# Optimization experiments

Hardware: AMD Instinct MI355X
Metric: run time of the kernel (lower is better)

## Reference

```python
import jax, jax.numpy as jnp
import numpy as np

N_NODES = 50000
N_EDGES = 800000
IN_F = 128
HID = 16
HEADS = 8
OUT_F = 128


def setup_inputs() -> dict:
    key = jax.random.key(0)
    ks = jax.random.split(key, 16)
    h = jax.random.normal(ks[0], (N_NODES, IN_F), dtype=jnp.float32)
    src1 = jax.random.randint(ks[1], (N_EDGES,), 0, N_NODES, dtype=jnp.int32)
    dst1 = jax.random.randint(ks[2], (N_EDGES,), 0, N_NODES, dtype=jnp.int32)
    src2 = jax.random.randint(ks[3], (N_EDGES,), 0, N_NODES, dtype=jnp.int32)
    dst2 = jax.random.randint(ks[4], (N_EDGES,), 0, N_NODES, dtype=jnp.int32)
    norm1 = jax.random.uniform(ks[5], (N_NODES, 1), dtype=jnp.float32)
    norm2 = jax.random.uniform(ks[6], (N_NODES, 1), dtype=jnp.float32)
    D = HEADS * HID  # 128
    W_lin = jax.random.normal(ks[7], (IN_F, D), dtype=jnp.float32) * (1.0 / np.sqrt(IN_F))
    b_lin = jax.random.normal(ks[8], (D,), dtype=jnp.float32) * 0.01
    al = jax.random.normal(ks[9], (HEADS, HID, 1), dtype=jnp.float32) * 0.1
    ar = jax.random.normal(ks[10], (HEADS, HID, 1), dtype=jnp.float32) * 0.1
    W_fc = jax.random.normal(ks[11], (D, OUT_F), dtype=jnp.float32) * (1.0 / np.sqrt(D))
    b_fc = jax.random.normal(ks[12], (OUT_F,), dtype=jnp.float32) * 0.01
    return {"h": h, "src1": src1, "dst1": dst1, "src2": src2, "dst2": dst2,
            "norm1": norm1, "norm2": norm2, "W_lin": W_lin, "b_lin": b_lin,
            "al": al, "ar": ar, "W_fc": W_fc, "b_fc": b_fc}


def _propagate(feat, norm, src, dst, n_nodes):
    # msg = h[src] * norm[src]; accum[v] = sum_{e: dst=v} msg_e; out = accum * norm
    msg = feat[src] * norm[src]                      # [E, D]
    agg = jax.ops.segment_sum(msg, dst, num_segments=n_nodes)
    return agg * norm                                # [N, D]


def _leaky_relu(x):
    return jnp.where(x > 0, x, 0.2 * x)


def reference(h, src1, dst1, src2, dst2, norm1, norm2, W_lin, b_lin, al, ar, W_fc, b_fc):
    N = h.shape[0]
    hf = h @ W_lin + b_lin                           # [N, 8*HID] (dropout p given but eval-mode -> identity)
    h1 = _propagate(hf, norm1, src1, dst1, N)
    h2 = _propagate(hf, norm2, src2, dst2, N)
    # Faithful to torch: row-major reshape [N, 8*HID] -> (8, N, HID)
    h1r = h1.reshape(HEADS, N, HID)
    h2r = h2.reshape(HEADS, N, HID)
    hr = hf.reshape(HEADS, N, HID)
    ai = jnp.einsum('hnd,hdo->hno', hr, al)          # [8, N, 1]
    aj1 = jnp.einsum('hnd,hdo->hno', h1r, ar)
    aj2 = jnp.einsum('hnd,hdo->hno', h2r, ar)
    a1 = jnp.clip(jnp.exp(_leaky_relu(ai + aj1)), -10.0, 10.0)
    a2 = jnp.clip(jnp.exp(_leaky_relu(ai + aj2)), -10.0, 10.0)
    denom = a1 + a2
    out = (a1 / denom) * h1r + (a2 / denom) * h2r    # [8, N, HID]
    out = out.reshape(N, HEADS * HID)
    return out @ W_fc + b_fc
```

## Files before the change

kernel.cpp:

```cpp
#include <hip/hip_runtime.h>

#define NN 50000
#define NE 800000
#define NB 196
#define NBLK 512
#define CHUNK 1563
#define MAXB 6144

typedef __bf16 bf16x8 __attribute__((ext_vector_type(8)));
typedef float  f32x4  __attribute__((ext_vector_type(4)));

__device__ __forceinline__ unsigned short f2bf(float x) {
    unsigned u = __float_as_uint(x);
    return (unsigned short)((u + 0x7FFFu + ((u >> 16) & 1u)) >> 16);
}
__device__ __forceinline__ float bflo(unsigned u) { return __uint_as_float(u << 16); }
__device__ __forceinline__ float bfhi(unsigned u) { return __uint_as_float(u & 0xFFFF0000u); }

__global__ __launch_bounds__(256) void convert_w_kernel(
    const float* __restrict__ Wa, const float* __restrict__ Wb,
    unsigned short* __restrict__ Wta, unsigned short* __restrict__ Wtb)
{
    __shared__ float ls[128 * 132];
    const float* W = blockIdx.x ? Wb : Wa;
    unsigned short* Wt = blockIdx.x ? Wtb : Wta;
    const int t = threadIdx.x;
    for (int i = t; i < 128 * 32; i += 256) {
        int k = i >> 5, n4 = i & 31;
        *(float4*)&ls[k * 132 + n4 * 4] = ((const float4*)W)[i];
    }
    __syncthreads();
    for (int j = t; j < 128 * 128; j += 256) {
        int n = j >> 7, k = j & 127;
        Wt[j] = f2bf(ls[k * 132 + n]);
    }
}

__global__ __launch_bounds__(256) void mfma_gemm_kernel(
    const float* __restrict__ X, const unsigned short* __restrict__ Wt,
    const float* __restrict__ bias, float* __restrict__ Y,
    unsigned short* __restrict__ Ybf, int nrows)
{
    __shared__ unsigned short Wl[128 * 128];
    const int t = threadIdx.x;
    const int lane = t & 63;
    const int wv = t >> 6;
    const int row0 = blockIdx.x * 64;
    const int m16 = lane & 15;
    const int quad = lane >> 4;

    {
        const uint4* Wg = (const uint4*)Wt;
        #pragma unroll
        for (int i = 0; i < 8; i++) {
            int gi = t + i * 256;
            int n = gi >> 4, g = gi & 15;
            uint4 v = Wg[gi];
            *(uint4*)&Wl[n * 128 + (((g ^ (n & 15)) << 3))] = v;
        }
    }

    const int arow = row0 + wv * 16 + m16;
    const bool valid = (arow < nrows);
    const float4* X4 = (const float4*)X;
    float4 xr[8];
    #pragma unroll
    for (int kc = 0; kc < 4; kc++) {
        if (valid) {
            int gidx = arow * 32 + kc * 8 + quad * 2;
            xr[kc * 2]     = X4[gidx];
            xr[kc * 2 + 1] = X4[gidx + 1];
        } else {
            xr[kc * 2] = xr[kc * 2 + 1] = make_float4(0.f, 0.f, 0.f, 0.f);
        }
    }
    __syncthreads();

    f32x4 acc[8];
    #pragma unroll
    for (int nt = 0; nt < 8; nt++) acc[nt] = (f32x4){0.f, 0.f, 0.f, 0.f};

    #pragma unroll
    for (int kc = 0; kc < 4; kc++) {
        union { unsigned short u[8]; bf16x8 v; } ah, al;
        float f[8] = { xr[kc*2].x, xr[kc*2].y, xr[kc*2].z, xr[kc*2].w,
                       xr[kc*2+1].x, xr[kc*2+1].y, xr[kc*2+1].z, xr[kc*2+1].w };
        #pragma unroll
        for (int j = 0; j < 8; j++) {
            unsigned u = __float_as_uint(f[j]);
            ah.u[j] = (unsigned short)(u >> 16);
            al.u[j] = f2bf(f[j] - __uint_as_float(u & 0xFFFF0000u));
        }
        const int sgbase = (kc * 4 + quad);
        #pragma unroll
        for (int nt = 0; nt < 8; nt++) {
            const int n = nt * 16 + m16;
            bf16x8 b = *(const bf16x8*)&Wl[n * 128 + ((sgbase ^ m16) << 3)];
            acc[nt] = __builtin_amdgcn_mfma_f32_16x16x32_bf16(ah.v, b, acc[nt], 0, 0, 0);
            acc[nt] = __builtin_amdgcn_mfma_f32_16x16x32_bf16(al.v, b, acc[nt], 0, 0, 0);
        }
    }

    #pragma unroll
    for (int nt = 0; nt < 8; nt++) {
        const int col = nt * 16 + m16;
        const float bc = bias[col];
        #pragma unroll
        for (int r = 0; r < 4; r++) {
            int row = row0 + wv * 16 + quad * 4 + r;
            if (row < nrows) {
                float val = acc[nt][r] + bc;
                if (Y)   Y[(long)row * 128 + col] = val;
                if (Ybf) Ybf[(long)row * 128 + col] = f2bf(val);
            }
        }
    }
}

__global__ __launch_bounds__(256) void histA_kernel(
    const int* __restrict__ dst1, const int* __restrict__ dst2, int* __restrict__ histG)
{
    __shared__ int h[2 * NB];
    const int t = threadIdx.x, blk = blockIdx.x;
    for (int i = t; i < 2 * NB; i += 256) h[i] = 0;
    __syncthreads();
    const int base = blk * CHUNK;
    const int lim = min(CHUNK, NE - base);
    for (int i = t; i < lim; i += 256) {
        atomicAdd(&h[dst1[base + i] >> 8], 1);
        atomicAdd(&h[NB + (dst2[base + i] >> 8)], 1);
    }
    __syncthreads();
    for (int i = t; i < 2 * NB; i += 256)
        histG[(size_t)i * NBLK + blk] = h[i];
}

__global__ __launch_bounds__(512) void scanB1_kernel(int* __restrict__ histG, int* __restrict__ btot)
{
    __shared__ int s[NBLK];
    const int t = threadIdx.x, row = blockIdx.x;
    int v = histG[(size_t)row * NBLK + t];
    s[t] = v;
    __syncthreads();
    for (int off = 1; off < NBLK; off <<= 1) {
        int x = (t >= off) ? s[t - off] : 0;
        __syncthreads();
        s[t] += x;
        __syncthreads();
    }
    histG[(size_t)row * NBLK + t] = s[t] - v;
    if (t == NBLK - 1) btot[row] = s[t];
}

__global__ __launch_bounds__(256) void scanB2_kernel(const int* __restrict__ btot, int* __restrict__ bbase)
{
    __shared__ int sc[256];
    const int t = threadIdx.x;
    for (int g = 0; g < 2; g++) {
        int v = (t < NB) ? btot[g * NB + t] : 0;
        sc[t] = v;
        __syncthreads();
        for (int off = 1; off < 256; off <<= 1) {
            int x = (t >= off) ? sc[t - off] : 0;
            __syncthreads();
            sc[t] += x;
            __syncthreads();
        }
        if (t < NB) bbase[g * NB + t] = sc[t] - v;
        __syncthreads();
    }
}

__global__ __launch_bounds__(256) void scatterC_kernel(
    const int* __restrict__ src1, const int* __restrict__ dst1,
    const int* __restrict__ src2, const int* __restrict__ dst2,
    const int* __restrict__ histG, const int* __restrict__ bbase,
    unsigned int* __restrict__ bin1, unsigned int* __restrict__ bin2)
{
    __shared__ int pos[2 * NB];
    const int t = threadIdx.x, blk = blockIdx.x;
    for (int i = t; i < 2 * NB; i += 256)
        pos[i] = bbase[i] + histG[(size_t)i * NBLK + blk];
    __syncthreads();
    const int base = blk * CHUNK;
    const int lim = min(CHUNK, NE - base);
    for (int i = t; i < lim; i += 256) {
        int d = dst1[base + i], s = src1[base + i];
        int slot = atomicAdd(&pos[d >> 8], 1);
        bin1[slot] = ((unsigned)(d & 255) << 16) | (unsigned)s;
        d = dst2[base + i]; s = src2[base + i];
        slot = atomicAdd(&pos[NB + (d >> 8)], 1);
        bin2[slot] = ((unsigned)(d & 255) << 16) | (unsigned)s;
    }
}

__global__ __launch_bounds__(256) void bucket_sort_kernel(
    const unsigned int* __restrict__ bin1, const unsigned int* __restrict__ bin2,
    const int* __restrict__ bbase, const int* __restrict__ btot,
    unsigned short* __restrict__ csr1, int* __restrict__ start1, int* __restrict__ deg1,
    unsigned short* __restrict__ csr2, int* __restrict__ start2, int* __restrict__ deg2)
{
    __shared__ int lcnt[256];
    __shared__ int sc[256];
    __shared__ int oat[256];
    __shared__ unsigned short outb[MAXB];
    const int t = threadIdx.x;
    const int g = (blockIdx.x >= NB) ? 1 : 0;
    const int b = blockIdx.x - g * NB;
    const unsigned int* bin = g ? bin2 : bin1;
    unsigned short* csr = g ? csr2 : csr1;
    int* start = g ? start2 : start1;
    int* deg   = g ? deg2 : deg1;

    const int base = bbase[g * NB + b];
    const int tot = min(btot[g * NB + b], MAXB);

    lcnt[t] = 0;
    __syncthreads();
    for (int i = t; i < tot; i += 256) atomicAdd(&lcnt[bin[base + i] >> 16], 1);
    __syncthreads();
    sc[t] = lcnt[t];
    __syncthreads();
    for (int off = 1; off < 256; off <<= 1) {
        int x = (t >= off) ? sc[t - off] : 0;
        __syncthreads();
        sc[t] += x;
        __syncthreads();
    }
    const int ex = sc[t] - lcnt[t];
    oat[t] = ex;
    __syncthreads();
    for (int i = t; i < tot; i += 256) {
        unsigned v = bin[base + i];
        int slot = atomicAdd(&oat[v >> 16], 1);
        outb[slot] = (unsigned short)(v & 0xFFFFu);
    }
    __syncthreads();
    for (int i = t; i < tot; i += 256) csr[base + i] = outb[i];
    int nd = b * 256 + t;
    if (nd < NN) { start[nd] = base + ex; deg[nd] = lcnt[t]; }
}

__global__ __launch_bounds__(256) void gather_both_kernel(
    const unsigned int* __restrict__ hfb,
    const unsigned short* __restrict__ csr1, const int* __restrict__ start1,
    const int* __restrict__ deg1, const float* __restrict__ norm1, float* __restrict__ agg1,
    const unsigned short* __restrict__ csr2, const int* __restrict__ start2,
    const int* __restrict__ deg2, const float* __restrict__ norm2, float* __restrict__ agg2)
{
    int w = (blockIdx.x * 256 + threadIdx.x) >> 6;
    int lane = threadIdx.x & 63;
    if (w >= 2 * NN) return;
    const int g = (w >= NN);
    const int node = w - g * NN;
    const unsigned short* csr = g ? csr2 : csr1;
    const int* start = g ? start2 : start1;
    const int* deg   = g ? deg2 : deg1;
    const float* norm = g ? norm2 : norm1;
    float* agg = g ? agg2 : agg1;

    int st = start[node];
    int dg = deg[node];
    float2 acc = make_float2(0.f, 0.f);
    int i = 0;
    for (; i + 4 <= dg; i += 4) {
        int s0 = csr[st + i], s1 = csr[st + i + 1], s2 = csr[st + i + 2], s3 = csr[st + i + 3];
        float n0 = norm[s0], n1 = norm[s1], n2 = norm[s2], n3 = norm[s3];
        unsigned u0 = hfb[(long)s0 * 64 + lane];
        unsigned u1 = hfb[(long)s1 * 64 + lane];
        unsigned u2 = hfb[(long)s2 * 64 + lane];
        unsigned u3 = hfb[(long)s3 * 64 + lane];
        acc.x = fmaf(bflo(u0), n0, acc.x); acc.y = fmaf(bfhi(u0), n0, acc.y);
        acc.x = fmaf(bflo(u1), n1, acc.x); acc.y = fmaf(bfhi(u1), n1, acc.y);
        acc.x = fmaf(bflo(u2), n2, acc.x); acc.y = fmaf(bfhi(u2), n2, acc.y);
        acc.x = fmaf(bflo(u3), n3, acc.x); acc.y = fmaf(bfhi(u3), n3, acc.y);
    }
    for (; i < dg; i++) {
        int s = csr[st + i];
        float nv = norm[s];
        unsigned u = hfb[(long)s * 64 + lane];
        acc.x = fmaf(bflo(u), nv, acc.x); acc.y = fmaf(bfhi(u), nv, acc.y);
    }
    ((float2*)agg)[(long)node * 64 + lane] = acc;
}

__global__ __launch_bounds__(256) void attention_kernel(
    const unsigned int* __restrict__ hfb, float* __restrict__ agg1,
    const float* __restrict__ agg2, const float* __restrict__ norm1,
    const float* __restrict__ norm2, const float* __restrict__ al,
    const float* __restrict__ ar)
{
    int gid = blockIdx.x * 256 + threadIdx.x;
    int m = gid >> 2;
    int j = gid & 3;
    if (m >= 8 * NN) return;
    int n = m >> 3;
    int head = m / NN;
    float n1 = norm1[n], n2v = norm2[n];
    uint2 u = ((const uint2*)hfb)[gid];
    float4 f = make_float4(bflo(u.x), bfhi(u.x), bflo(u.y), bfhi(u.y));
    float4 g1 = ((const float4*)agg1)[gid];
    float4 g2 = ((const float4*)agg2)[gid];
    g1.x *= n1; g1.y *= n1; g1.z *= n1; g1.w *= n1;
    g2.x *= n2v; g2.y *= n2v; g2.z *= n2v; g2.w *= n2v;
    float4 av = ((const float4*)al)[head * 4 + j];
    float4 rv = ((const float4*)ar)[head * 4 + j];
    float s_ai = f.x * av.x + f.y * av.y + f.z * av.z + f.w * av.w;
    float s1 = g1.x * rv.x + g1.y * rv.y + g1.z * rv.z + g1.w * rv.w;
    float s2 = g2.x * rv.x + g2.y * rv.y + g2.z * rv.z + g2.w * rv.w;
    s_ai += __shfl_xor(s_ai, 1); s_ai += __shfl_xor(s_ai, 2);
    s1   += __shfl_xor(s1, 1);   s1   += __shfl_xor(s1, 2);
    s2   += __shfl_xor(s2, 1);   s2   += __shfl_xor(s2, 2);
    float x1 = s_ai + s1; x1 = x1 > 0.f ? x1 : 0.2f * x1;
    float x2 = s_ai + s2; x2 = x2 > 0.f ? x2 : 0.2f * x2;
    float e1 = fminf(expf(x1), 10.f);
    float e2 = fminf(expf(x2), 10.f);
    float inv = 1.f / (e1 + e2);
    float w1 = e1 * inv, w2 = e2 * inv;
    float4 o;
    o.x = w1 * g1.x + w2 * g2.x;
    o.y = w1 * g1.y + w2 * g2.y;
    o.z = w1 * g1.z + w2 * g2.z;
    o.w = w1 * g1.w + w2 * g2.w;
    ((float4*)agg1)[gid] = o;
}

extern "C" void kernel_launch(void* const* d_in, const int* in_sizes, int n_in,
                              void* d_out, int out_size, void* d_ws, size_t ws_size,
                              hipStream_t stream)
{
    const float* h     = (const float*)d_in[0];
    const int*   src1  = (const int*)  d_in[1];
    const int*   dst1  = (const int*)  d_in[2];
    const int*   src2  = (const int*)  d_in[3];
    const int*   dst2  = (const int*)  d_in[4];
    const float* norm1 = (const float*)d_in[5];
    const float* norm2 = (const float*)d_in[6];
    const float* W_lin = (const float*)d_in[7];
    const float* b_lin = (const float*)d_in[8];
    const float* al    = (const float*)d_in[9];
    const float* ar    = (const float*)d_in[10];
    const float* W_fc  = (const float*)d_in[11];
    const float* b_fc  = (const float*)d_in[12];
    float* out = (float*)d_out;

    float* agg1 = (float*)d_ws;
    float* agg2 = agg1 + (size_t)NN * 128;
    unsigned int* bin1 = (unsigned int*)agg2;
    unsigned int* bin2 = bin1 + NE;
    unsigned short* hfb  = (unsigned short*)(agg2 + (size_t)NN * 128);
    unsigned short* csr1 = hfb + (size_t)NN * 128;
    unsigned short* csr2 = csr1 + NE;
    unsigned short* WtL  = csr2 + NE;
    unsigned short* WtF  = WtL + 128 * 128;
    int* histG  = (int*)(WtF + 128 * 128);
    int* btot   = histG + 2 * NB * NBLK;
    int* bbase  = btot + 2 * NB;
    int* start1 = bbase + 2 * NB;
    int* start2 = start1 + NN;
    int* deg1   = start2 + NN;
    int* deg2   = deg1 + NN;

    convert_w_kernel<<<2, 256, 0, stream>>>(W_lin, W_fc, WtL, WtF);

    mfma_gemm_kernel<<<(NN + 63) / 64, 256, 0, stream>>>(h, WtL, b_lin, nullptr, hfb, NN);

    histA_kernel<<<NBLK, 256, 0, stream>>>(dst1, dst2, histG);
    scanB1_kernel<<<2 * NB, NBLK, 0, stream>>>(histG, btot);
    scanB2_kernel<<<1, 256, 0, stream>>>(btot, bbase);
    scatterC_kernel<<<NBLK, 256, 0, stream>>>(src1, dst1, src2, dst2, histG, bbase, bin1, bin2);
    bucket_sort_kernel<<<2 * NB, 256, 0, stream>>>(bin1, bin2, bbase, btot,
                                                   csr1, start1, deg1,
                                                   csr2, start2, deg2);

    gather_both_kernel<<<(2 * NN * 64 + 255) / 256, 256, 0, stream>>>(
        (const unsigned int*)hfb,
        csr1, start1, deg1, norm1, agg1,
        csr2, start2, deg2, norm2, agg2);

    attention_kernel<<<8 * NN * 4 / 256, 256, 0, stream>>>((const unsigned int*)hfb, agg1, agg2,
                                                           norm1, norm2, al, ar);

    mfma_gemm_kernel<<<(NN + 63) / 64, 256, 0, stream>>>(agg1, WtF, b_fc, out, nullptr, NN);
}
```

Before: 262.1 us.

## Fuse gather with attention and feed bf16 output to single-pass GEMM

Merges the two-graph gather and the attention step into one kernel, where one wavefront handles a node for both graphs. CSR indices are loaded cooperatively and broadcast with readlane. The fp32 agg1/agg2 intermediates are no longer written and reread; attention output goes out as bf16. The final GEMM reads that bf16 tensor with a single MFMA pass instead of the split hi/lo passes on fp32 input. This cuts memory traffic and launches, but it lowers the precision of the FC input to plain bf16.

After: 229.3 us. -12.5%, faster.

```diff
diff --git a/kernel.cpp b/kernel.cpp
--- a/kernel.cpp
+++ b/kernel.cpp
@@ -113,6 +113,67 @@
                 if (Y)   Y[(long)row * 128 + col] = val;
                 if (Ybf) Ybf[(long)row * 128 + col] = f2bf(val);
             }
+        }
+    }
+}
+
+__global__ __launch_bounds__(256) void mfma_gemm_bf16_kernel(
+    const unsigned short* __restrict__ Xbf, const unsigned short* __restrict__ Wt,
+    const float* __restrict__ bias, float* __restrict__ Y, int nrows)
+{
+    __shared__ unsigned short Wl[128 * 128];
+    const int t = threadIdx.x;
+    const int lane = t & 63;
+    const int wv = t >> 6;
+    const int row0 = blockIdx.x * 64;
+    const int m16 = lane & 15;
+    const int quad = lane >> 4;
+
+    {
+        const uint4* Wg = (const uint4*)Wt;
+        #pragma unroll
+        for (int i = 0; i < 8; i++) {
+            int gi = t + i * 256;
+            int n = gi >> 4, g = gi & 15;
+            uint4 v = Wg[gi];
+            *(uint4*)&Wl[n * 128 + (((g ^ (n & 15)) << 3))] = v;
+        }
+    }
+
+    const int arow = row0 + wv * 16 + m16;
+    const bool valid = (arow < nrows);
+    const uint4* X16 = (const uint4*)Xbf;
+    union { uint4 u; bf16x8 v; } xr[4];
+    #pragma unroll
+    for (int kc = 0; kc < 4; kc++) {
+        if (valid) xr[kc].u = X16[arow * 16 + kc * 4 + quad];
+        else       xr[kc].u = make_uint4(0, 0, 0, 0);
+    }
+    __syncthreads();
+
+    f32x4 acc[8];
+    #pragma unroll
+    for (int nt = 0; nt < 8; nt++) acc[nt] = (f32x4){0.f, 0.f, 0.f, 0.f};
+
+    #pragma unroll
+    for (int kc = 0; kc < 4; kc++) {
+        const int sgbase = (kc * 4 + quad);
+        #pragma unroll
+        for (int nt = 0; nt < 8; nt++) {
+            const int n = nt * 16 + m16;
+            bf16x8 b = *(const bf16x8*)&Wl[n * 128 + ((sgbase ^ m16) << 3)];
+            acc[nt] = __builtin_amdgcn_mfma_f32_16x16x32_bf16(xr[kc].v, b, acc[nt], 0, 0, 0);
+        }
+    }
+
+    #pragma unroll
+    for (int nt = 0; nt < 8; nt++) {
+        const int col = nt * 16 + m16;
+        const float bc = bias[col];
+        #pragma unroll
+        for (int r = 0; r < 4; r++) {
+            int row = row0 + wv * 16 + quad * 4 + r;
+            if (row < nrows) Y[(long)row * 128 + col] = acc[nt][r] + bc;
         }
     }
 }
@@ -241,88 +302,108 @@
     if (nd < NN) { start[nd] = base + ex; deg[nd] = lcnt[t]; }
 }
 
-__global__ __launch_bounds__(256) void gather_both_kernel(
+__global__ __launch_bounds__(256) void gather_attn_kernel(
     const unsigned int* __restrict__ hfb,
     const unsigned short* __restrict__ csr1, const int* __restrict__ start1,
-    const int* __restrict__ deg1, const float* __restrict__ norm1, float* __restrict__ agg1,
+    const int* __restrict__ deg1, const float* __restrict__ norm1,
     const unsigned short* __restrict__ csr2, const int* __restrict__ start2,
-    const int* __restrict__ deg2, const float* __restrict__ norm2, float* __restrict__ agg2)
-{
-    int w = (blockIdx.x * 256 + threadIdx.x) >> 6;
-    int lane = threadIdx.x & 63;
-    if (w >= 2 * NN) return;
-    const int g = (w >= NN);
-    const int node = w - g * NN;
-    const unsigned short* csr = g ? csr2 : csr1;
-    const int* start = g ? start2 : start1;
-    const int* deg   = g ? deg2 : deg1;
-    const float* norm = g ? norm2 : norm1;
-    float* agg = g ? agg2 : agg1;
-
-    int st = start[node];
-    int dg = deg[node];
-    float2 acc = make_float2(0.f, 0.f);
-    int i = 0;
-    for (; i + 4 <= dg; i += 4) {
-        int s0 = csr[st + i], s1 = csr[st + i + 1], s2 = csr[st + i + 2], s3 = csr[st + i + 3];
-        float n0 = norm[s0], n1 = norm[s1], n2 = norm[s2], n3 = norm[s3];
-        unsigned u0 = hfb[(long)s0 * 64 + lane];
-        unsigned u1 = hfb[(long)s1 * 64 + lane];
-        unsigned u2 = hfb[(long)s2 * 64 + lane];
-        unsigned u3 = hfb[(long)s3 * 64 + lane];
-        acc.x = fmaf(bflo(u0), n0, acc.x); acc.y = fmaf(bfhi(u0), n0, acc.y);
-        acc.x = fmaf(bflo(u1), n1, acc.x); acc.y = fmaf(bfhi(u1), n1, acc.y);
-        acc.x = fmaf(bflo(u2), n2, acc.x); acc.y = fmaf(bfhi(u2), n2, acc.y);
-        acc.x = fmaf(bflo(u3), n3, acc.x); acc.y = fmaf(bfhi(u3), n3, acc.y);
-    }
-    for (; i < dg; i++) {
-        int s = csr[st + i];
-        float nv = norm[s];
-        unsigned u = hfb[(long)s * 64 + lane];
-        acc.x = fmaf(bflo(u), nv, acc.x); acc.y = fmaf(bfhi(u), nv, acc.y);
-    }
-    ((float2*)agg)[(long)node * 64 + lane] = acc;
-}
-
-__global__ __launch_bounds__(256) void attention_kernel(
-    const unsigned int* __restrict__ hfb, float* __restrict__ agg1,
-    const float* __restrict__ agg2, const float* __restrict__ norm1,
-    const float* __restrict__ norm2, const float* __restrict__ al,
-    const float* __restrict__ ar)
-{
-    int gid = blockIdx.x * 256 + threadIdx.x;
-    int m = gid >> 2;
-    int j = gid & 3;
-    if (m >= 8 * NN) return;
-    int n = m >> 3;
-    int head = m / NN;
-    float n1 = norm1[n], n2v = norm2[n];
-    uint2 u = ((const uint2*)hfb)[gid];
-    float4 f = make_float4(bflo(u.x), bfhi(u.x), bflo(u.y), bfhi(u.y));
-    float4 g1 = ((const float4*)agg1)[gid];
-    float4 g2 = ((const float4*)agg2)[gid];
-    g1.x *= n1; g1.y *= n1; g1.z *= n1; g1.w *= n1;
-    g2.x *= n2v; g2.y *= n2v; g2.z *= n2v; g2.w *= n2v;
-    float4 av = ((const float4*)al)[head * 4 + j];
-    float4 rv = ((const float4*)ar)[head * 4 + j];
-    float s_ai = f.x * av.x + f.y * av.y + f.z * av.z + f.w * av.w;
-    float s1 = g1.x * rv.x + g1.y * rv.y + g1.z * rv.z + g1.w * rv.w;
-    float s2 = g2.x * rv.x + g2.y * rv.y + g2.z * rv.z + g2.w * rv.w;
-    s_ai += __shfl_xor(s_ai, 1); s_ai += __shfl_xor(s_ai, 2);
-    s1   += __shfl_xor(s1, 1);   s1   += __shfl_xor(s1, 2);
-    s2   += __shfl_xor(s2, 1);   s2   += __shfl_xor(s2, 2);
+    const int* __restrict__ deg2, const float* __restrict__ norm2,
+    const float* __restrict__ al, const float* __restrict__ ar,
+    unsigned int* __restrict__ outb)
+{
+    const int lane = threadIdx.x & 63;
+    int node = (blockIdx.x * 256 + threadIdx.x) >> 6;
+    if (node >= NN) return;
+    node = __builtin_amdgcn_readfirstlane(node);
+
+    float2 acc1 = make_float2(0.f, 0.f), acc2 = make_float2(0.f, 0.f);
+
+    {
+        const int st = start1[node], dg = deg1[node];
+        for (int base = 0; base < dg; base += 64) {
+            const int nb = min(64, dg - base);
+            int myc = (lane < nb) ? (int)csr1[st + base + lane] : 0;
+            int j = 0;
+            for (; j + 4 <= nb; j += 4) {
+                int s0 = __builtin_amdgcn_readlane(myc, j);
+                int s1 = __builtin_amdgcn_readlane(myc, j + 1);
+                int s2 = __builtin_amdgcn_readlane(myc, j + 2);
+                int s3 = __builtin_amdgcn_readlane(myc, j + 3);
+                float n0 = norm1[s0], n1 = norm1[s1], n2 = norm1[s2], n3 = norm1[s3];
+                unsigned u0 = hfb[(long)s0 * 64 + lane];
+                unsigned u1 = hfb[(long)s1 * 64 + lane];
+                unsigned u2 = hfb[(long)s2 * 64 + lane];
+                unsigned u3 = hfb[(long)s3 * 64 + lane];
+                acc1.x = fmaf(bflo(u0), n0, acc1.x); acc1.y = fmaf(bfhi(u0), n0, acc1.y);
+                acc1.x = fmaf(bflo(u1), n1, acc1.x); acc1.y = fmaf(bfhi(u1), n1, acc1.y);
+                acc1.x = fmaf(bflo(u2), n2, acc1.x); acc1.y = fmaf(bfhi(u2), n2, acc1.y);
+                acc1.x = fmaf(bflo(u3), n3, acc1.x); acc1.y = fmaf(bfhi(u3), n3, acc1.y);
+            }
+            for (; j < nb; j++) {
+                int s = __builtin_amdgcn_readlane(myc, j);
+                float nv = norm1[s];
+                unsigned u = hfb[(long)s * 64 + lane];
+                acc1.x = fmaf(bflo(u), nv, acc1.x); acc1.y = fmaf(bfhi(u), nv, acc1.y);
+            }
+        }
+    }
+    {
+        const int st = start2[node], dg = deg2[node];
+        for (int base = 0; base < dg; base += 64) {
+            const int nb = min(64, dg - base);
+            int myc = (lane < nb) ? (int)csr2[st + base + lane] : 0;
+            int j = 0;
+            for (; j + 4 <= nb; j += 4) {
+                int s0 = __builtin_amdgcn_readlane(myc, j);
+                int s1 = __builtin_amdgcn_readlane(myc, j + 1);
+                int s2 = __builtin_amdgcn_readlane(myc, j + 2);
+                int s3 = __builtin_amdgcn_readlane(myc, j + 3);
+                float n0 = norm2[s0], n1 = norm2[s1], n2 = norm2[s2], n3 = norm2[s3];
+                unsigned u0 = hfb[(long)s0 * 64 + lane];
+                unsigned u1 = hfb[(long)s1 * 64 + lane];
+                unsigned u2 = hfb[(long)s2 * 64 + lane];
+                unsigned u3 = hfb[(long)s3 * 64 + lane];
+                acc2.x = fmaf(bflo(u0), n0, acc2.x); acc2.y = fmaf(bfhi(u0), n0, acc2.y);
+                acc2.x = fmaf(bflo(u1), n1, acc2.x); acc2.y = fmaf(bfhi(u1), n1, acc2.y);
+                acc2.x = fmaf(bflo(u2), n2, acc2.x); acc2.y = fmaf(bfhi(u2), n2, acc2.y);
+                acc2.x = fmaf(bflo(u3), n3, acc2.x); acc2.y = fmaf(bfhi(u3), n3, acc2.y);
+            }
+            for (; j < nb; j++) {
+                int s = __builtin_amdgcn_readlane(myc, j);
+                float nv = norm2[s];
+                unsigned u = hfb[(long)s * 64 + lane];
+                acc2.x = fmaf(bflo(u), nv, acc2.x); acc2.y = fmaf(bfhi(u), nv, acc2.y);
+            }
+        }
+    }
+
+    const float nn1 = norm1[node], nn2 = norm2[node];
+    acc1.x *= nn1; acc1.y *= nn1;
+    acc2.x *= nn2; acc2.y *= nn2;
+
+    const int cc = lane >> 3;
+    const int m = node * 8 + cc;
+    const int head = m / NN;
+    const int hid = (2 * lane) & 15;
+    unsigned uf = hfb[(long)node * 64 + lane];
+    const float fx = bflo(uf), fy = bfhi(uf);
+    const float av0 = al[head * 16 + hid], av1 = al[head * 16 + hid + 1];
+    const float rv0 = ar[head * 16 + hid], rv1 = ar[head * 16 + hid + 1];
+    float s_ai = fx * av0 + fy * av1;
+    float s1 = acc1.x * rv0 + acc1.y * rv1;
+    float s2 = acc2.x * rv0 + acc2.y * rv1;
+    s_ai += __shfl_xor(s_ai, 1); s_ai += __shfl_xor(s_ai, 2); s_ai += __shfl_xor(s_ai, 4);
+    s1   += __shfl_xor(s1, 1);   s1   += __shfl_xor(s1, 2);   s1   += __shfl_xor(s1, 4);
+    s2   += __shfl_xor(s2, 1);   s2   += __shfl_xor(s2, 2);   s2   += __shfl_xor(s2, 4);
     float x1 = s_ai + s1; x1 = x1 > 0.f ? x1 : 0.2f * x1;
     float x2 = s_ai + s2; x2 = x2 > 0.f ? x2 : 0.2f * x2;
     float e1 = fminf(expf(x1), 10.f);
     float e2 = fminf(expf(x2), 10.f);
     float inv = 1.f / (e1 + e2);
     float w1 = e1 * inv, w2 = e2 * inv;
-    float4 o;
-    o.x = w1 * g1.x + w2 * g2.x;
-    o.y = w1 * g1.y + w2 * g2.y;
-    o.z = w1 * g1.z + w2 * g2.z;
-    o.w = w1 * g1.w + w2 * g2.w;
-    ((float4*)agg1)[gid] = o;
+    float ox = w1 * acc1.x + w2 * acc2.x;
+    float oy = w1 * acc1.y + w2 * acc2.y;
+    outb[(long)node * 64 + lane] = (unsigned)f2bf(ox) | ((unsigned)f2bf(oy) << 16);
 }
 
 extern "C" void kernel_launch(void* const* d_in, const int* in_sizes, int n_in,
@@ -344,12 +425,11 @@
     const float* b_fc  = (const float*)d_in[12];
     float* out = (float*)d_out;
 
-    float* agg1 = (float*)d_ws;
-    float* agg2 = agg1 + (size_t)NN * 128;
-    unsigned int* bin1 = (unsigned int*)agg2;
+    unsigned short* hfb  = (unsigned short*)d_ws;
+    unsigned short* outbf = hfb + (size_t)NN * 128;
+    unsigned int* bin1 = (unsigned int*)(outbf + (size_t)NN * 128);
     unsigned int* bin2 = bin1 + NE;
-    unsigned short* hfb  = (unsigned short*)(agg2 + (size_t)NN * 128);
-    unsigned short* csr1 = hfb + (size_t)NN * 128;
+    unsigned short* csr1 = (unsigned short*)(bin2 + NE);
     unsigned short* csr2 = csr1 + NE;
     unsigned short* WtL  = csr2 + NE;
     unsigned short* WtF  = WtL + 128 * 128;
@@ -373,13 +453,11 @@
                                                    csr1, start1, deg1,
                                                    csr2, start2, deg2);
 
-    gather_both_kernel<<<(2 * NN * 64 + 255) / 256, 256, 0, stream>>>(
+    gather_attn_kernel<<<(NN * 64 + 255) / 256, 256, 0, stream>>>(
         (const unsigned int*)hfb,
-        csr1, start1, deg1, norm1, agg1,
-        csr2, start2, deg2, norm2, agg2);
-
-    attention_kernel<<<8 * NN * 4 / 256, 256, 0, stream>>>((const unsigned int*)hfb, agg1, agg2,
-                                                           norm1, norm2, al, ar);
-
-    mfma_gemm_kernel<<<(NN + 63) / 64, 256, 0, stream>>>(agg1, WtF, b_fc, out, nullptr, NN);
-}
+        csr1, start1, deg1, norm1,
+        csr2, start2, deg2, norm2,
+        al, ar, (unsigned int*)outbf);
+
+    mfma_gemm_bf16_kernel<<<(NN + 63) / 64, 256, 0, stream>>>(outbf, WtF, b_fc, out, NN);
+}
```
